# Performance work log

Measured on AMD Instinct MI355X. Metric: run time of the kernel, lower is better.

The kernel has to match this reference:

```python
import jax, jax.numpy as jnp
import numpy as np
import math

NEG = -1e9  # finite stand-in for -inf under masking (exactly zeroed by entmax support)

def entmax15(z):
    # Exact 1.5-entmax along last axis (Peters et al. 2019, sort-based).
    z = z / 2.0
    z = z - jnp.max(z, axis=-1, keepdims=True)            # shift-invariant
    zs = -jnp.sort(-z, axis=-1)                            # descending sort
    L = zs.shape[-1]
    k = jnp.arange(1, L + 1, dtype=z.dtype)
    mean = jnp.cumsum(zs, axis=-1) / k                     # running mean
    mean_sq = jnp.cumsum(zs * zs, axis=-1) / k             # running mean of squares
    ss = k * (mean_sq - mean * mean)
    delta = (1.0 - ss) / k
    tau = mean - jnp.sqrt(jnp.clip(delta, 0.0))
    support_size = jnp.sum(tau <= zs, axis=-1, keepdims=True)  # k*
    tau_star = jnp.take_along_axis(tau, support_size - 1, axis=-1)
    p = jnp.square(jnp.clip(z - tau_star, 0.0))
    return p

def setup_inputs() -> dict:
    key = jax.random.key(0)
    ks = jax.random.split(key, 7)
    B, L, D = 2, 1536, 768
    query = jax.random.normal(ks[0], (B, L, D), dtype=jnp.float32)
    kee = jax.random.normal(ks[1], (B, L, D), dtype=jnp.float32)
    mask = jax.random.randint(ks[2], (B, L), 0, 2, dtype=jnp.int32)
    s = 1.0 / math.sqrt(D)
    wq_w = jax.random.uniform(ks[3], (D, D), jnp.float32, -s, s)
    wq_b = jax.random.uniform(ks[4], (D,), jnp.float32, -s, s)
    wk_w = jax.random.uniform(ks[5], (D, D), jnp.float32, -s, s)
    wk_b = jax.random.uniform(ks[6], (D,), jnp.float32, -s, s)
    return {"query": query, "key": kee, "mask": mask,
            "wq_w": wq_w, "wq_b": wq_b, "wk_w": wk_w, "wk_b": wk_b}

def reference(query, key, mask, wq_w, wq_b, wk_w, wk_b):
    B, Lq, D = query.shape
    H = 12
    dk = D // H
    q = (query @ wq_w.T + wq_b).reshape(B, Lq, H, dk)
    k = (key @ wk_w.T + wk_b).reshape(B, -1, H, dk)
    # scores: [B, H, Lq, Lk]
    scores = jnp.einsum('bqhd,bkhd->bhqk', q, k) / math.sqrt(dk)
    kpm = (mask != 0)[:, None, None, :]                    # key padding mask
    scores = jnp.where(kpm, scores, NEG)
    p_attn = entmax15(scores)
    return jnp.sum(p_attn, axis=1) / H                     # [B, Lq, Lk]
```

## Files before the change

kernel.cpp:

```cpp
#include <hip/hip_runtime.h>
#include <math.h>

#define BB 2
#define LL 1536
#define DD 768
#define HH 12
#define DKK 64
#define ZNEG -5.0e8f

typedef __attribute__((ext_vector_type(8))) short bf16x8;
typedef __attribute__((ext_vector_type(8))) unsigned short u16x8;
typedef __attribute__((ext_vector_type(4))) float f32x4;

__device__ __forceinline__ unsigned short f32_to_bf16_rn(float x) {
    unsigned int u = __float_as_uint(x);
    u += 0x7fffu + ((u >> 16) & 1u);
    return (unsigned short)(u >> 16);
}
__device__ __forceinline__ float bf16u_to_f32(unsigned short h) {
    return __uint_as_float(((unsigned int)h) << 16);
}

__device__ __forceinline__ void split8(const float* __restrict__ gsrc,
                                       unsigned short* __restrict__ hdst,
                                       unsigned short* __restrict__ ldst) {
    float4 v0 = *reinterpret_cast<const float4*>(gsrc);
    float4 v1 = *reinterpret_cast<const float4*>(gsrc + 4);
    float f[8] = {v0.x, v0.y, v0.z, v0.w, v1.x, v1.y, v1.z, v1.w};
    u16x8 hi, lo;
    #pragma unroll
    for (int i = 0; i < 8; ++i) {
        unsigned short h = f32_to_bf16_rn(f[i]);
        float r = f[i] - bf16u_to_f32(h);
        hi[i] = h;
        lo[i] = f32_to_bf16_rn(r);
    }
    *reinterpret_cast<u16x8*>(hdst) = hi;
    *reinterpret_cast<u16x8*>(ldst) = lo;
}

__global__ __launch_bounds__(256) void proj_mfma(
    const float* __restrict__ Xq, const float* __restrict__ Xk,
    const float* __restrict__ Wq, const float* __restrict__ Wk,
    const float* __restrict__ bq, const float* __restrict__ bk,
    float* __restrict__ Qp, float* __restrict__ Kp)
{
    const float* X    = blockIdx.z ? Xk : Xq;
    const float* W    = blockIdx.z ? Wk : Wq;
    const float* bias = blockIdx.z ? bk : bq;
    float*       Out  = blockIdx.z ? Kp : Qp;

    __shared__ alignas(16) unsigned short Ah[8 * 64 * 8];
    __shared__ alignas(16) unsigned short Al[8 * 64 * 8];
    __shared__ alignas(16) unsigned short Bh[4 * 64 * 8];
    __shared__ alignas(16) unsigned short Bl[4 * 64 * 8];

    const int tid  = threadIdx.x;
    const int lane = tid & 63;
    const int w    = tid >> 6;
    const int wm   = w & 1;
    const int wn   = w >> 1;
    const int m0   = blockIdx.y * 128;
    const int n0   = blockIdx.x * 64;

    f32x4 acc[4][2] = {};

    for (int k0 = 0; k0 < DD; k0 += 32) {
        #pragma unroll
        for (int i = 0; i < 2; ++i) {
            const int c = tid + (i << 8);
            const int m = c >> 2, g = c & 3;
            const int slot = ((m >> 4) * 64 + (m & 15) + (g << 4)) * 8;
            split8(X + (size_t)(m0 + m) * DD + k0 + g * 8, Ah + slot, Al + slot);
        }
        {
            const int n = tid >> 2, g = tid & 3;
            const int slot = ((n >> 4) * 64 + (n & 15) + (g << 4)) * 8;
            split8(W + (size_t)(n0 + n) * DD + k0 + g * 8, Bh + slot, Bl + slot);
        }
        __syncthreads();

        bf16x8 aH[4], aL[4], bH[2], bL[2];
        #pragma unroll
        for (int fm = 0; fm < 4; ++fm) {
            const int f = wm * 4 + fm;
            aH[fm] = *reinterpret_cast<const bf16x8*>(Ah + (f * 64 + lane) * 8);
            aL[fm] = *reinterpret_cast<const bf16x8*>(Al + (f * 64 + lane) * 8);
        }
        #pragma unroll
        for (int fn = 0; fn < 2; ++fn) {
            const int f = wn * 2 + fn;
            bH[fn] = *reinterpret_cast<const bf16x8*>(Bh + (f * 64 + lane) * 8);
            bL[fn] = *reinterpret_cast<const bf16x8*>(Bl + (f * 64 + lane) * 8);
        }
        #pragma unroll
        for (int fm = 0; fm < 4; ++fm)
            #pragma unroll
            for (int fn = 0; fn < 2; ++fn) {
                acc[fm][fn] = __builtin_amdgcn_mfma_f32_16x16x32_bf16(aH[fm], bH[fn], acc[fm][fn], 0, 0, 0);
                acc[fm][fn] = __builtin_amdgcn_mfma_f32_16x16x32_bf16(aH[fm], bL[fn], acc[fm][fn], 0, 0, 0);
                acc[fm][fn] = __builtin_amdgcn_mfma_f32_16x16x32_bf16(aL[fm], bH[fn], acc[fm][fn], 0, 0, 0);
            }
        __syncthreads();
    }

    const int r0 = (lane >> 4) << 2;
    const int cl = lane & 15;
    #pragma unroll
    for (int fn = 0; fn < 2; ++fn) {
        const int col = n0 + wn * 32 + fn * 16 + cl;
        const float bv = bias[col];
        #pragma unroll
        for (int fm = 0; fm < 4; ++fm) {
            const int row = m0 + wm * 64 + fm * 16 + r0;
            #pragma unroll
            for (int r = 0; r < 4; ++r)
                Out[(size_t)(row + r) * DD + col] = acc[fm][fn][r] + bv;
        }
    }
}

__global__ __launch_bounds__(256) void scores_mfma(
    const float* __restrict__ Qp, const float* __restrict__ Kp,
    const int* __restrict__ mask, float* __restrict__ S)
{
    const int bh = blockIdx.z;
    const int b  = bh / HH;
    const int h  = bh - b * HH;
    const int q0 = blockIdx.y * 128;
    const int n0 = blockIdx.x * 64;

    __shared__ alignas(16) unsigned short Ah[8 * 2 * 64 * 8];
    __shared__ alignas(16) unsigned short Al[8 * 2 * 64 * 8];
    __shared__ alignas(16) unsigned short Bh[4 * 2 * 64 * 8];
    __shared__ alignas(16) unsigned short Bl[4 * 2 * 64 * 8];

    const int tid  = threadIdx.x;
    const int lane = tid & 63;
    const int w    = tid >> 6;
    const int wm   = w & 1;
    const int wn   = w >> 1;

    #pragma unroll
    for (int i = 0; i < 4; ++i) {
        const int c = tid + (i << 8);
        const int m = c >> 3, c8 = c & 7;
        const int qq = c8 >> 2, g = c8 & 3;
        const int slot = (((m >> 4) * 2 + qq) * 64 + (m & 15) + (g << 4)) * 8;
        split8(Qp + (size_t)(b * LL + q0 + m) * DD + h * DKK + c8 * 8, Ah + slot, Al + slot);
    }
    #pragma unroll
    for (int i = 0; i < 2; ++i) {
        const int c = tid + (i << 8);
        const int n = c >> 3, c8 = c & 7;
        const int qq = c8 >> 2, g = c8 & 3;
        const int slot = (((n >> 4) * 2 + qq) * 64 + (n & 15) + (g << 4)) * 8;
        split8(Kp + (size_t)(b * LL + n0 + n) * DD + h * DKK + c8 * 8, Bh + slot, Bl + slot);
    }
    __syncthreads();

    f32x4 acc[4][2] = {};
    #pragma unroll
    for (int qq = 0; qq < 2; ++qq) {
        bf16x8 aH[4], aL[4], bH[2], bL[2];
        #pragma unroll
        for (int fm = 0; fm < 4; ++fm) {
            const int f = (wm * 4 + fm) * 2 + qq;
            aH[fm] = *reinterpret_cast<const bf16x8*>(Ah + (f * 64 + lane) * 8);
            aL[fm] = *reinterpret_cast<const bf16x8*>(Al + (f * 64 + lane) * 8);
        }
        #pragma unroll
        for (int fn = 0; fn < 2; ++fn) {
            const int f = (wn * 2 + fn) * 2 + qq;
            bH[fn] = *reinterpret_cast<const bf16x8*>(Bh + (f * 64 + lane) * 8);
            bL[fn] = *reinterpret_cast<const bf16x8*>(Bl + (f * 64 + lane) * 8);
        }
        #pragma unroll
        for (int fm = 0; fm < 4; ++fm)
            #pragma unroll
            for (int fn = 0; fn < 2; ++fn) {
                acc[fm][fn] = __builtin_amdgcn_mfma_f32_16x16x32_bf16(aH[fm], bH[fn], acc[fm][fn], 0, 0, 0);
                acc[fm][fn] = __builtin_amdgcn_mfma_f32_16x16x32_bf16(aH[fm], bL[fn], acc[fm][fn], 0, 0, 0);
                acc[fm][fn] = __builtin_amdgcn_mfma_f32_16x16x32_bf16(aL[fm], bH[fn], acc[fm][fn], 0, 0, 0);
            }
    }

    const int r0 = (lane >> 4) << 2;
    const int cl = lane & 15;
    #pragma unroll
    for (int fn = 0; fn < 2; ++fn) {
        const int col = n0 + wn * 32 + fn * 16 + cl;
        const int mk  = mask[b * LL + col];
        #pragma unroll
        for (int fm = 0; fm < 4; ++fm) {
            const int row = q0 + wm * 64 + fm * 16 + r0;
            const size_t base = ((size_t)bh * LL + row) * LL + col;
            #pragma unroll
            for (int r = 0; r < 4; ++r) {
                const float v = acc[fm][fn][r] * 0.0625f;
                S[base + (size_t)r * LL] = mk ? v : ZNEG;
            }
        }
    }
}

__device__ __forceinline__ float waveReduceSum(float v) {
    #pragma unroll
    for (int off = 32; off > 0; off >>= 1) v += __shfl_xor(v, off, 64);
    return v;
}
__device__ __forceinline__ float waveReduceMax(float v) {
    #pragma unroll
    for (int off = 32; off > 0; off >>= 1) v = fmaxf(v, __shfl_xor(v, off, 64));
    return v;
}

__global__ __launch_bounds__(256) void entmax_sum(
    const float* __restrict__ S, float* __restrict__ out)
{
    const int bq = blockIdx.x;
    const int b  = bq / LL;
    const int q  = bq - b * LL;
    const int tid = threadIdx.x;
    const int w  = tid >> 6;
    const int l  = tid & 63;

    __shared__ float buf[4][LL];

    float acc[24];
    #pragma unroll
    for (int i = 0; i < 24; ++i) acc[i] = 0.0f;

    #pragma unroll
    for (int hi = 0; hi < 3; ++hi) {
        const int h = w + (hi << 2);
        const float* row = S + ((size_t)(b * HH + h) * LL + q) * LL + l * 24;

        float z[24];
        #pragma unroll
        for (int i = 0; i < 24; i += 4) {
            float4 v = *reinterpret_cast<const float4*>(row + i);
            z[i] = v.x; z[i + 1] = v.y; z[i + 2] = v.z; z[i + 3] = v.w;
        }

        float m = z[0];
        #pragma unroll
        for (int i = 1; i < 24; ++i) m = fmaxf(m, z[i]);
        m = waveReduceMax(m);

        #pragma unroll
        for (int i = 0; i < 24; ++i) z[i] -= m;

        float lo = -1.0f, hi_ = 0.0f;
        for (int it = 0; it < 16; ++it) {
            const float tau = 0.5f * (lo + hi_);
            float s = 0.0f;
            #pragma unroll
            for (int i = 0; i < 24; ++i) {
                const float t = fmaxf(z[i] - tau, 0.0f);
                s = fmaf(t, t, s);
            }
            s = waveReduceSum(s);
            if (s >= 1.0f) lo = tau; else hi_ = tau;
        }
        const float tau = 0.5f * (lo + hi_);

        #pragma unroll
        for (int i = 0; i < 24; ++i) {
            const float t = fmaxf(z[i] - tau, 0.0f);
            acc[i] = fmaf(t, t, acc[i]);
        }
    }

    #pragma unroll
    for (int i = 0; i < 24; ++i) buf[w][l * 24 + i] = acc[i];
    __syncthreads();

    float* orow = out + (size_t)bq * LL;
    #pragma unroll
    for (int i = 0; i < 6; ++i) {
        const int c = tid + (i << 8);
        orow[c] = (buf[0][c] + buf[1][c] + buf[2][c] + buf[3][c]) * (1.0f / 12.0f);
    }
}

extern "C" void kernel_launch(void* const* d_in, const int* in_sizes, int n_in,
                              void* d_out, int out_size, void* d_ws, size_t ws_size,
                              hipStream_t stream) {
    (void)in_sizes; (void)n_in; (void)out_size; (void)ws_size;
    const float* query = (const float*)d_in[0];
    const float* key   = (const float*)d_in[1];
    const int*   mask  = (const int*)d_in[2];
    const float* wq_w  = (const float*)d_in[3];
    const float* wq_b  = (const float*)d_in[4];
    const float* wk_w  = (const float*)d_in[5];
    const float* wk_b  = (const float*)d_in[6];
    float* out = (float*)d_out;

    float* Qp = (float*)d_ws;
    float* Kp = Qp + (size_t)BB * LL * DD;
    float* S  = Kp + (size_t)BB * LL * DD;

    proj_mfma<<<dim3(DD / 64, (BB * LL) / 128, 2), 256, 0, stream>>>(
        query, key, wq_w, wk_w, wq_b, wk_b, Qp, Kp);

    scores_mfma<<<dim3(LL / 64, LL / 128, BB * HH), 256, 0, stream>>>(
        Qp, Kp, mask, S);

    entmax_sum<<<BB * LL, 256, 0, stream>>>(S, out);
}
```

Baseline: 253.7 us.

## Emit bf16 hi/lo from projection, load MFMA frags directly, compact entmax candidates

The projection kernel now writes Q and K as split bf16 hi/lo pairs, so the scores kernel no longer re-splits them. Instead of staging through shared memory, the scores kernel loads MFMA fragments straight from global memory. The entmax kernel keeps only entries above -1 (the only ones that can be in the support, since tau lies in [-1,0]), packs them into shared memory with a prefix-sum, and runs the bisection over this smaller set, using a register-only path when at most 128 survive. This cuts reduction work per bisection step but adds block barriers and shared memory traffic, and the projection now does scattered 2-byte stores.

```diff
diff --git a/kernel.cpp b/kernel.cpp
--- a/kernel.cpp
+++ b/kernel.cpp
@@ -43,12 +43,14 @@
     const float* __restrict__ Xq, const float* __restrict__ Xk,
     const float* __restrict__ Wq, const float* __restrict__ Wk,
     const float* __restrict__ bq, const float* __restrict__ bk,
-    float* __restrict__ Qp, float* __restrict__ Kp)
+    unsigned short* __restrict__ Qh, unsigned short* __restrict__ Ql,
+    unsigned short* __restrict__ Kh, unsigned short* __restrict__ Kl)
 {
     const float* X    = blockIdx.z ? Xk : Xq;
     const float* W    = blockIdx.z ? Wk : Wq;
     const float* bias = blockIdx.z ? bk : bq;
-    float*       Out  = blockIdx.z ? Kp : Qp;
+    unsigned short* Oh = blockIdx.z ? Kh : Qh;
+    unsigned short* Ol = blockIdx.z ? Kl : Ql;
 
     __shared__ alignas(16) unsigned short Ah[8 * 64 * 8];
     __shared__ alignas(16) unsigned short Al[8 * 64 * 8];
@@ -114,14 +116,21 @@
         for (int fm = 0; fm < 4; ++fm) {
             const int row = m0 + wm * 64 + fm * 16 + r0;
             #pragma unroll
-            for (int r = 0; r < 4; ++r)
-                Out[(size_t)(row + r) * DD + col] = acc[fm][fn][r] + bv;
+            for (int r = 0; r < 4; ++r) {
+                const float v = acc[fm][fn][r] + bv;
+                const unsigned short h16 = f32_to_bf16_rn(v);
+                const float res = v - bf16u_to_f32(h16);
+                const size_t o = (size_t)(row + r) * DD + col;
+                Oh[o] = h16;
+                Ol[o] = f32_to_bf16_rn(res);
+            }
         }
     }
 }
 
 __global__ __launch_bounds__(256) void scores_mfma(
-    const float* __restrict__ Qp, const float* __restrict__ Kp,
+    const unsigned short* __restrict__ Qh, const unsigned short* __restrict__ Ql,
+    const unsigned short* __restrict__ Kh, const unsigned short* __restrict__ Kl,
     const int* __restrict__ mask, float* __restrict__ S)
 {
     const int bh = blockIdx.z;
@@ -130,50 +139,33 @@
     const int q0 = blockIdx.y * 128;
     const int n0 = blockIdx.x * 64;
 
-    __shared__ alignas(16) unsigned short Ah[8 * 2 * 64 * 8];
-    __shared__ alignas(16) unsigned short Al[8 * 2 * 64 * 8];
-    __shared__ alignas(16) unsigned short Bh[4 * 2 * 64 * 8];
-    __shared__ alignas(16) unsigned short Bl[4 * 2 * 64 * 8];
-
     const int tid  = threadIdx.x;
     const int lane = tid & 63;
     const int w    = tid >> 6;
     const int wm   = w & 1;
     const int wn   = w >> 1;
-
-    #pragma unroll
-    for (int i = 0; i < 4; ++i) {
-        const int c = tid + (i << 8);
-        const int m = c >> 3, c8 = c & 7;
-        const int qq = c8 >> 2, g = c8 & 3;
-        const int slot = (((m >> 4) * 2 + qq) * 64 + (m & 15) + (g << 4)) * 8;
-        split8(Qp + (size_t)(b * LL + q0 + m) * DD + h * DKK + c8 * 8, Ah + slot, Al + slot);
-    }
-    #pragma unroll
-    for (int i = 0; i < 2; ++i) {
-        const int c = tid + (i << 8);
-        const int n = c >> 3, c8 = c & 7;
-        const int qq = c8 >> 2, g = c8 & 3;
-        const int slot = (((n >> 4) * 2 + qq) * 64 + (n & 15) + (g << 4)) * 8;
-        split8(Kp + (size_t)(b * LL + n0 + n) * DD + h * DKK + c8 * 8, Bh + slot, Bl + slot);
-    }
-    __syncthreads();
+    const int lr   = lane & 15;
+    const int lk   = lane >> 4;
+
+    const size_t abase = (size_t)(b * LL + q0 + wm * 64 + lr) * DD + h * DKK + lk * 8;
+    const size_t bbase = (size_t)(b * LL + n0 + wn * 32 + lr) * DD + h * DKK + lk * 8;
 
     f32x4 acc[4][2] = {};
+
     #pragma unroll
     for (int qq = 0; qq < 2; ++qq) {
         bf16x8 aH[4], aL[4], bH[2], bL[2];
         #pragma unroll
         for (int fm = 0; fm < 4; ++fm) {
-            const int f = (wm * 4 + fm) * 2 + qq;
-            aH[fm] = *reinterpret_cast<const bf16x8*>(Ah + (f * 64 + lane) * 8);
-            aL[fm] = *reinterpret_cast<const bf16x8*>(Al + (f * 64 + lane) * 8);
+            const size_t o = abase + (size_t)fm * 16 * DD + qq * 32;
+            aH[fm] = *reinterpret_cast<const bf16x8*>(Qh + o);
+            aL[fm] = *reinterpret_cast<const bf16x8*>(Ql + o);
         }
         #pragma unroll
         for (int fn = 0; fn < 2; ++fn) {
-            const int f = (wn * 2 + fn) * 2 + qq;
-            bH[fn] = *reinterpret_cast<const bf16x8*>(Bh + (f * 64 + lane) * 8);
-            bL[fn] = *reinterpret_cast<const bf16x8*>(Bl + (f * 64 + lane) * 8);
+            const size_t o = bbase + (size_t)fn * 16 * DD + qq * 32;
+            bH[fn] = *reinterpret_cast<const bf16x8*>(Kh + o);
+            bL[fn] = *reinterpret_cast<const bf16x8*>(Kl + o);
         }
         #pragma unroll
         for (int fm = 0; fm < 4; ++fm)
@@ -232,8 +224,8 @@
     for (int i = 0; i < 24; ++i) acc[i] = 0.0f;
 
     #pragma unroll
-    for (int hi = 0; hi < 3; ++hi) {
-        const int h = w + (hi << 2);
+    for (int hh = 0; hh < 3; ++hh) {
+        const int h = w + (hh << 2);
         const float* row = S + ((size_t)(b * HH + h) * LL + q) * LL + l * 24;
 
         float z[24];
@@ -247,24 +239,53 @@
         #pragma unroll
         for (int i = 1; i < 24; ++i) m = fmaxf(m, z[i]);
         m = waveReduceMax(m);
-
         #pragma unroll
         for (int i = 0; i < 24; ++i) z[i] -= m;
 
-        float lo = -1.0f, hi_ = 0.0f;
-        for (int it = 0; it < 16; ++it) {
-            const float tau = 0.5f * (lo + hi_);
-            float s = 0.0f;
-            #pragma unroll
-            for (int i = 0; i < 24; ++i) {
-                const float t = fmaxf(z[i] - tau, 0.0f);
-                s = fmaf(t, t, s);
-            }
-            s = waveReduceSum(s);
-            if (s >= 1.0f) lo = tau; else hi_ = tau;
-        }
-        const float tau = 0.5f * (lo + hi_);
-
+        int nloc = 0;
+        #pragma unroll
+        for (int i = 0; i < 24; ++i) nloc += (z[i] > -1.0f) ? 1 : 0;
+        int incl = nloc;
+        #pragma unroll
+        for (int off = 1; off <= 32; off <<= 1) {
+            int t = __shfl_up(incl, off, 64);
+            if (l >= off) incl += t;
+        }
+        const int ntot = __shfl(incl, 63, 64);
+
+        int p = incl - nloc;
+        #pragma unroll
+        for (int i = 0; i < 24; ++i)
+            if (z[i] > -1.0f) buf[w][p++] = z[i];
+        __syncthreads();
+
+        float tlo = -1.0f, thi = 0.0f;
+        if (ntot <= 128) {
+            float x0 = (l < ntot)      ? buf[w][l]      : -2.0f;
+            float x1 = (l + 64 < ntot) ? buf[w][l + 64] : -2.0f;
+            for (int it = 0; it < 16; ++it) {
+                const float tau = 0.5f * (tlo + thi);
+                const float t0 = fmaxf(x0 - tau, 0.0f);
+                const float t1 = fmaxf(x1 - tau, 0.0f);
+                float s = fmaf(t0, t0, t1 * t1);
+                s = waveReduceSum(s);
+                if (s >= 1.0f) tlo = tau; else thi = tau;
+            }
+        } else {
+            for (int it = 0; it < 16; ++it) {
+                const float tau = 0.5f * (tlo + thi);
+                float s = 0.0f;
+                for (int j = l; j < ntot; j += 64) {
+                    const float t = fmaxf(buf[w][j] - tau, 0.0f);
+                    s = fmaf(t, t, s);
+                }
+                s = waveReduceSum(s);
+                if (s >= 1.0f) tlo = tau; else thi = tau;
+            }
+        }
+        __syncthreads();
+
+        const float tau = 0.5f * (tlo + thi);
         #pragma unroll
         for (int i = 0; i < 24; ++i) {
             const float t = fmaxf(z[i] - tau, 0.0f);
@@ -297,15 +318,18 @@
     const float* wk_b  = (const float*)d_in[6];
     float* out = (float*)d_out;
 
-    float* Qp = (float*)d_ws;
-    float* Kp = Qp + (size_t)BB * LL * DD;
-    float* S  = Kp + (size_t)BB * LL * DD;
+    const size_t NE = (size_t)BB * LL * DD;
+    unsigned short* Qh = (unsigned short*)d_ws;
+    unsigned short* Ql = Qh + NE;
+    unsigned short* Kh = Ql + NE;
+    unsigned short* Kl = Kh + NE;
+    float* S = (float*)(Kl + NE);
 
     proj_mfma<<<dim3(DD / 64, (BB * LL) / 128, 2), 256, 0, stream>>>(
-        query, key, wq_w, wk_w, wq_b, wk_b, Qp, Kp);
+        query, key, wq_w, wk_w, wq_b, wk_b, Qh, Ql, Kh, Kl);
 
     scores_mfma<<<dim3(LL / 64, LL / 128, BB * HH), 256, 0, stream>>>(
-        Qp, Kp, mask, S);
+        Qh, Ql, Kh, Kl, mask, S);
 
     entmax_sum<<<BB * LL, 256, 0, stream>>>(S, out);
 }
```

After: 347.5 us. 1.37x slower.
